# Optimization experiments

Hardware: AMD Instinct MI355X
Metric: run time of the kernel (lower is better)

Reference implementation:

```python
import math
import jax, jax.numpy as jnp
import numpy as np

C = 256
CQ = C // 8
B, H, W = 8, 64, 64


def setup_inputs() -> dict:
    key = jax.random.key(0)
    k1, k2, k3, k4 = jax.random.split(key, 4)
    x = jax.random.normal(k1, (B, C, H, W), dtype=jnp.float32)
    # 1x1 conv weights, bias=False -> plain [out, in] matrices
    wq = jax.random.normal(k2, (CQ, C), dtype=jnp.float32) * 0.02
    wk = jax.random.normal(k3, (CQ, C), dtype=jnp.float32) * 0.02
    wv = jax.random.normal(k4, (C, C), dtype=jnp.float32) * 0.02
    # gamma init is zeros in the torch module; use small nonzero so output depends on attention path
    gamma = jnp.ones((1,), dtype=jnp.float32) * 0.5
    return {"x": x, "wq": wq, "wk": wk, "wv": wv, "gamma": gamma}


def reference(x, wq, wk, wv, gamma):
    b, c, h, w = x.shape
    n = h * w
    xr = x.reshape(b, c, n)                       # [B, C, N]
    q = jnp.einsum('oc,bcn->bon', wq, xr)         # [B, Cq, N]
    k = jnp.einsum('oc,bcn->bon', wk, xr)         # [B, Cq, N]
    v = jnp.einsum('oc,bcn->bon', wv, xr)         # [B, C, N]
    # attn[b, i, j] = softmax_j( q[:, i] . k[:, j] / sqrt(Cq) )
    scores = jnp.einsum('bci,bcj->bij', q, k) / math.sqrt(q.shape[1])  # [B, N, N]
    attn = jax.nn.softmax(scores, axis=-1)
    # out[b, c, m] = sum_n v[b, c, n] * attn[b, m, n]
    out = jnp.einsum('bcn,bmn->bcm', v, attn).reshape(b, c, h, w)
    return gamma[0] * out + x
```

## Files before the change

kernel.cpp:

```cpp
#include <hip/hip_runtime.h>

#define B_ 8
#define C_ 256
#define CQ_ 32
#define N_ 4096

typedef __attribute__((ext_vector_type(8))) short short8;
typedef __attribute__((ext_vector_type(4))) float float4v;

#define QSCALE 0.2550599232f

#if __has_builtin(__builtin_amdgcn_exp2f)
#define EXP2F __builtin_amdgcn_exp2f
#else
#define EXP2F exp2f
#endif

static __device__ __forceinline__ unsigned short f2bf(float f) {
  unsigned int u = __float_as_uint(f);
  u += 0x7FFFu + ((u >> 16) & 1u);
  return (unsigned short)(u >> 16);
}

static __device__ __forceinline__ void async16(void* lds, const void* g) {
  __builtin_amdgcn_global_load_lds(
      (const __attribute__((address_space(1))) unsigned int*)g,
      (__attribute__((address_space(3))) unsigned int*)lds, 16, 0, 0);
}

__global__ __launch_bounds__(256) void wconv_kernel(
    const float* __restrict__ wq, const float* __restrict__ wk,
    const float* __restrict__ wv, unsigned short* __restrict__ w_bf) {
  int o = blockIdx.x * 8 + (threadIdx.x >> 5);
  int c8 = (threadIdx.x & 31) * 8;
  const float* src; float sc = 1.f;
  if (o < 32)      { src = wq + (size_t)o * 256; sc = QSCALE; }
  else if (o < 64) { src = wk + (size_t)(o - 32) * 256; }
  else             { src = wv + (size_t)(o - 64) * 256; }
  float4 a = *(const float4*)(src + c8);
  float4 bq = *(const float4*)(src + c8 + 4);
  unsigned short t[8] = {f2bf(a.x*sc), f2bf(a.y*sc), f2bf(a.z*sc), f2bf(a.w*sc),
                         f2bf(bq.x*sc), f2bf(bq.y*sc), f2bf(bq.z*sc), f2bf(bq.w*sc)};
  *(uint4*)(w_bf + (size_t)o * 256 + c8) = *(const uint4*)t;
}

__global__ __launch_bounds__(256, 2) void proj_kernel(
    const float* __restrict__ x, const unsigned short* __restrict__ w_bf,
    unsigned short* __restrict__ qT, unsigned short* __restrict__ kT,
    unsigned short* __restrict__ v) {
  __shared__ __align__(16) unsigned short xb[2][64 * 32];
  int tid = threadIdx.x, wave = tid >> 6, lane = tid & 63;
  int q16 = lane >> 4, l16 = lane & 15;
  int b = blockIdx.x, n0 = blockIdx.y * 64;

  int p = tid & 15, n4g = tid >> 4;
  const float* x0 = x + (size_t)b * C_ * N_ + n0 + n4g * 4;

  auto stage = [&](int buf, int ks) {
    const float* r0 = x0 + (size_t)(ks * 32 + 2 * p) * N_;
    float4 fa = *(const float4*)(r0);
    float4 fb = *(const float4*)(r0 + N_);
    float va[4] = {fa.x, fa.y, fa.z, fa.w};
    float vb[4] = {fb.x, fb.y, fb.z, fb.w};
    #pragma unroll
    for (int i = 0; i < 4; ++i) {
      int n = n4g * 4 + i;
      unsigned int pk = (unsigned int)f2bf(va[i]) | ((unsigned int)f2bf(vb[i]) << 16);
      int so = (p >> 2) ^ ((n >> 1) & 3);
      *(unsigned int*)(&xb[buf][n * 32 + so * 8 + (p & 3) * 2]) = pk;
    }
  };

  float4v acc[5][4];
  float4v zerov = {0.f, 0.f, 0.f, 0.f};
  #pragma unroll
  for (int mt = 0; mt < 5; ++mt)
    for (int nt = 0; nt < 4; ++nt) acc[mt][nt] = zerov;

  stage(0, 0);
  __syncthreads();

  int o0 = wave * 80;
  int sxo = (q16 ^ ((l16 >> 1) & 3)) * 8;
  #pragma unroll 1
  for (int ks = 0; ks < 8; ++ks) {
    if (ks < 7) stage((ks + 1) & 1, ks + 1);
    short8 af[5], bf4[4];
    #pragma unroll
    for (int mt = 0; mt < 5; ++mt)
      af[mt] = *(const short8*)(w_bf + (size_t)(o0 + mt * 16 + l16) * 256 + ks * 32 + q16 * 8);
    #pragma unroll
    for (int nt = 0; nt < 4; ++nt)
      bf4[nt] = *(const short8*)(&xb[ks & 1][(nt * 16 + l16) * 32 + sxo]);
    #pragma unroll
    for (int mt = 0; mt < 5; ++mt)
      #pragma unroll
      for (int nt = 0; nt < 4; ++nt)
        acc[mt][nt] = __builtin_amdgcn_mfma_f32_16x16x32_bf16(af[mt], bf4[nt], acc[mt][nt], 0, 0, 0);
    __syncthreads();
  }

  #pragma unroll
  for (int mt = 0; mt < 5; ++mt) {
    int og = o0 + mt * 16 + q16 * 4;
    #pragma unroll
    for (int nt = 0; nt < 4; ++nt) {
      int n = n0 + nt * 16 + l16;
      unsigned short t[4];
      if (og < 64) {
        #pragma unroll
        for (int r = 0; r < 4; ++r) t[r] = f2bf(acc[mt][nt][r]);
        unsigned short* dst = (og < 32) ? (qT + ((size_t)b * N_ + n) * CQ_ + og)
                                        : (kT + ((size_t)b * N_ + n) * CQ_ + (og - 32));
        *(uint2*)dst = *(const uint2*)t;
      } else {
        #pragma unroll
        for (int r = 0; r < 4; ++r)
          v[((size_t)b * C_ + og - 64 + r) * N_ + n] = f2bf(acc[mt][nt][r]);
      }
    }
  }
}

__global__ __launch_bounds__(256, 2) void attn_kernel(
    const unsigned short* __restrict__ qT, const unsigned short* __restrict__ kT,
    const unsigned short* __restrict__ v, const float* __restrict__ x,
    const float* __restrict__ gamma, float* __restrict__ out) {
  __shared__ __align__(16) unsigned short kt_lds[2][64 * 32];
  __shared__ __align__(16) unsigned short p_lds[2][64 * 64];
  __shared__ float l_lds[64];

  int tid = threadIdx.x, wave = tid >> 6, lane = tid & 63;
  int q16 = lane >> 4, l16 = lane & 15;
  int bid = blockIdx.x, b = bid & 7, m0 = (bid >> 3) * 64;

  short8 qfrag = *(const short8*)(qT + ((size_t)b * N_ + m0 + wave * 16 + l16) * CQ_ + q16 * 8);

  auto stageK = [&](int buf, int j0) {
    int r = wave * 16 + (lane >> 2);
    int lo = (lane & 3) ^ ((r >> 1) & 3);
    async16(&kt_lds[buf][wave * 16 * 32], kT + ((size_t)b * N_ + j0 + r) * CQ_ + lo * 8);
  };

  const unsigned short* vw = v + ((size_t)b * C_ + wave * 64) * N_;
  uint4 vfr[2][8];
  auto vload = [&](uint4* dst, int j0) {
    #pragma unroll
    for (int ks = 0; ks < 2; ++ks)
      #pragma unroll
      for (int ct = 0; ct < 4; ++ct)
        dst[ks * 4 + ct] =
            *(const uint4*)(vw + (size_t)(ct * 16 + l16) * N_ + j0 + ks * 32 + q16 * 8);
  };

  stageK(0, 0);
  __syncthreads();
  vload(vfr[0], 0);

  float4v acc[4][4];
  float4v zerov = {0.f, 0.f, 0.f, 0.f};
  #pragma unroll
  for (int mt = 0; mt < 4; ++mt)
    for (int ct = 0; ct < 4; ++ct) acc[mt][ct] = zerov;
  float lrun[4] = {0.f, 0.f, 0.f, 0.f};

  int kro = q16 ^ ((l16 >> 1) & 3);
  int vro = l16 & 7;
  int lo8 = l16 >> 3, li = l16 & 7;

  #pragma unroll 2
  for (int j = 0; j < 64; ++j) {
    int cur = j & 1;
    float4v s[4];
    #pragma unroll
    for (int jt = 0; jt < 4; ++jt) {
      short8 kf = *(const short8*)(&kt_lds[cur][(jt * 16 + l16) * 32 + kro * 8]);
      s[jt] = __builtin_amdgcn_mfma_f32_16x16x32_bf16(qfrag, kf, zerov, 0, 0, 0);
    }
    if (j < 63) stageK(cur ^ 1, (j + 1) * 64);

    #pragma unroll
    for (int r = 0; r < 4; ++r) {
      float p0 = EXP2F(s[0][r]), p1 = EXP2F(s[1][r]);
      float p2 = EXP2F(s[2][r]), p3 = EXP2F(s[3][r]);
      lrun[r] += (p0 + p1) + (p2 + p3);
      int prow = wave * 16 + q16 * 4 + r;
      int rl = (q16 * 4 + r) & 7;
      unsigned short* pr = &p_lds[cur][prow * 64 + li];
      int o0 = lo8 ^ rl;
      pr[(o0 ^ 0) * 8] = (unsigned short)(__float_as_uint(p0) >> 16);
      pr[(o0 ^ 2) * 8] = (unsigned short)(__float_as_uint(p1) >> 16);
      pr[(o0 ^ 4) * 8] = (unsigned short)(__float_as_uint(p2) >> 16);
      pr[(o0 ^ 6) * 8] = (unsigned short)(__float_as_uint(p3) >> 16);
    }
    if (j == 63) {
      #pragma unroll
      for (int r = 0; r < 4; ++r) {
        float t = lrun[r];
        t += __shfl_xor(t, 1); t += __shfl_xor(t, 2);
        t += __shfl_xor(t, 4); t += __shfl_xor(t, 8);
        if (l16 == 0) l_lds[wave * 16 + q16 * 4 + r] = t;
      }
    }
    __syncthreads();

    if (j < 63) vload(vfr[cur ^ 1], (j + 1) * 64);

    #pragma unroll
    for (int ks = 0; ks < 2; ++ks) {
      short8 pf[4];
      #pragma unroll
      for (int mt = 0; mt < 4; ++mt)
        pf[mt] = *(const short8*)(&p_lds[cur][(mt * 16 + l16) * 64 + ((ks * 4 + q16) ^ vro) * 8]);
      #pragma unroll
      for (int ct = 0; ct < 4; ++ct) {
        short8 vf = *(const short8*)&vfr[cur][ks * 4 + ct];
        #pragma unroll
        for (int mt = 0; mt < 4; ++mt)
          acc[mt][ct] = __builtin_amdgcn_mfma_f32_16x16x32_bf16(pf[mt], vf, acc[mt][ct], 0, 0, 0);
      }
    }
  }

  float g = gamma[0];
  #pragma unroll
  for (int mt = 0; mt < 4; ++mt) {
    float linv[4];
    #pragma unroll
    for (int r = 0; r < 4; ++r) linv[r] = 1.f / l_lds[mt * 16 + q16 * 4 + r];
    int n = m0 + mt * 16 + q16 * 4;
    #pragma unroll
    for (int ct = 0; ct < 4; ++ct) {
      int c = wave * 64 + ct * 16 + l16;
      size_t off = ((size_t)b * C_ + c) * N_ + n;
      float4 xv = *(const float4*)(x + off);
      float4 o;
      o.x = g * acc[mt][ct][0] * linv[0] + xv.x;
      o.y = g * acc[mt][ct][1] * linv[1] + xv.y;
      o.z = g * acc[mt][ct][2] * linv[2] + xv.z;
      o.w = g * acc[mt][ct][3] * linv[3] + xv.w;
      *(float4*)(out + off) = o;
    }
  }
}

extern "C" void kernel_launch(void* const* d_in, const int* in_sizes, int n_in,
                              void* d_out, int out_size, void* d_ws, size_t ws_size,
                              hipStream_t stream) {
  const float* x     = (const float*)d_in[0];
  const float* wq    = (const float*)d_in[1];
  const float* wk    = (const float*)d_in[2];
  const float* wv    = (const float*)d_in[3];
  const float* gamma = (const float*)d_in[4];
  float* out = (float*)d_out;

  unsigned short* qT  = (unsigned short*)d_ws;
  unsigned short* kT  = qT + (size_t)B_ * N_ * CQ_;
  unsigned short* vv  = kT + (size_t)B_ * N_ * CQ_;
  unsigned short* wbf = vv + (size_t)B_ * C_ * N_;

  hipLaunchKernelGGL(wconv_kernel, dim3(40), dim3(256), 0, stream, wq, wk, wv, wbf);
  hipLaunchKernelGGL(proj_kernel, dim3(8, 64), dim3(256), 0, stream, x, wbf, qT, kT, vv);
  hipLaunchKernelGGL(attn_kernel, dim3(512), dim3(256), 0, stream, qT, kT, vv, x, gamma, out);
}
```

Before: 228.6 us.

## Double attention block to 128 query rows with V staged in shared LDS

Each attention block now covers 128 query rows with 512 threads (8 waves), halving the grid. Each V tile is staged once into LDS via async copies and shared by both halves of the query rows, so V is fetched from global memory half as often as before, when every wave loaded its own V fragments into registers. In exchange the P buffer is single-buffered and a second __syncthreads per iteration guards the V and P LDS reuse, which serialises more of the loop. The larger LDS footprint and block size may also lower occupancy, and 256 blocks may underfill the GPU.

```diff
diff --git a/kernel.cpp b/kernel.cpp
--- a/kernel.cpp
+++ b/kernel.cpp
@@ -122,40 +122,42 @@
   }
 }
 
-__global__ __launch_bounds__(256, 2) void attn_kernel(
+__global__ __launch_bounds__(512, 2) void attn_kernel(
     const unsigned short* __restrict__ qT, const unsigned short* __restrict__ kT,
     const unsigned short* __restrict__ v, const float* __restrict__ x,
     const float* __restrict__ gamma, float* __restrict__ out) {
+  __shared__ __align__(16) unsigned short v_lds[256 * 64];
   __shared__ __align__(16) unsigned short kt_lds[2][64 * 32];
-  __shared__ __align__(16) unsigned short p_lds[2][64 * 64];
-  __shared__ float l_lds[64];
+  __shared__ __align__(16) unsigned short p_lds[128 * 64];
+  __shared__ float l_lds[128];
 
   int tid = threadIdx.x, wave = tid >> 6, lane = tid & 63;
   int q16 = lane >> 4, l16 = lane & 15;
-  int bid = blockIdx.x, b = bid & 7, m0 = (bid >> 3) * 64;
+  int bid = blockIdx.x, b = bid & 7, m0 = (bid >> 3) * 128;
 
   short8 qfrag = *(const short8*)(qT + ((size_t)b * N_ + m0 + wave * 16 + l16) * CQ_ + q16 * 8);
 
+  const unsigned short* vbase = v + (size_t)b * C_ * N_;
+  auto stageV = [&](int j0) {
+    #pragma unroll
+    for (int it = 0; it < 4; ++it) {
+      int r = wave * 32 + it * 8 + (lane >> 3);
+      int lo = (lane & 7) ^ (lane >> 3);
+      async16(&v_lds[(wave * 32 + it * 8) * 64], vbase + (size_t)r * N_ + j0 + lo * 8);
+    }
+  };
   auto stageK = [&](int buf, int j0) {
-    int r = wave * 16 + (lane >> 2);
-    int lo = (lane & 3) ^ ((r >> 1) & 3);
-    async16(&kt_lds[buf][wave * 16 * 32], kT + ((size_t)b * N_ + j0 + r) * CQ_ + lo * 8);
+    if (wave >= 4) {
+      int w4 = wave - 4;
+      int r = w4 * 16 + (lane >> 2);
+      int lo = (lane & 3) ^ ((r >> 1) & 3);
+      async16(&kt_lds[buf][w4 * 16 * 32], kT + ((size_t)b * N_ + j0 + r) * CQ_ + lo * 8);
+    }
   };
 
-  const unsigned short* vw = v + ((size_t)b * C_ + wave * 64) * N_;
-  uint4 vfr[2][8];
-  auto vload = [&](uint4* dst, int j0) {
-    #pragma unroll
-    for (int ks = 0; ks < 2; ++ks)
-      #pragma unroll
-      for (int ct = 0; ct < 4; ++ct)
-        dst[ks * 4 + ct] =
-            *(const uint4*)(vw + (size_t)(ct * 16 + l16) * N_ + j0 + ks * 32 + q16 * 8);
-  };
-
   stageK(0, 0);
+  stageV(0);
   __syncthreads();
-  vload(vfr[0], 0);
 
   float4v acc[4][4];
   float4v zerov = {0.f, 0.f, 0.f, 0.f};
@@ -167,8 +169,8 @@
   int kro = q16 ^ ((l16 >> 1) & 3);
   int vro = l16 & 7;
   int lo8 = l16 >> 3, li = l16 & 7;
-
-  #pragma unroll 2
+  int h = wave >> 2, cq = wave & 3;
+
   for (int j = 0; j < 64; ++j) {
     int cur = j & 1;
     float4v s[4];
@@ -177,7 +179,6 @@
       short8 kf = *(const short8*)(&kt_lds[cur][(jt * 16 + l16) * 32 + kro * 8]);
       s[jt] = __builtin_amdgcn_mfma_f32_16x16x32_bf16(qfrag, kf, zerov, 0, 0, 0);
     }
-    if (j < 63) stageK(cur ^ 1, (j + 1) * 64);
 
     #pragma unroll
     for (int r = 0; r < 4; ++r) {
@@ -186,7 +187,7 @@
       lrun[r] += (p0 + p1) + (p2 + p3);
       int prow = wave * 16 + q16 * 4 + r;
       int rl = (q16 * 4 + r) & 7;
-      unsigned short* pr = &p_lds[cur][prow * 64 + li];
+      unsigned short* pr = &p_lds[prow * 64 + li];
       int o0 = lo8 ^ rl;
       pr[(o0 ^ 0) * 8] = (unsigned short)(__float_as_uint(p0) >> 16);
       pr[(o0 ^ 2) * 8] = (unsigned short)(__float_as_uint(p1) >> 16);
@@ -204,22 +205,26 @@
     }
     __syncthreads();
 
-    if (j < 63) vload(vfr[cur ^ 1], (j + 1) * 64);
+    if (j < 63) stageK(cur ^ 1, (j + 1) * 64);
 
     #pragma unroll
     for (int ks = 0; ks < 2; ++ks) {
-      short8 pf[4];
+      short8 pf[4], vf[4];
       #pragma unroll
       for (int mt = 0; mt < 4; ++mt)
-        pf[mt] = *(const short8*)(&p_lds[cur][(mt * 16 + l16) * 64 + ((ks * 4 + q16) ^ vro) * 8]);
-      #pragma unroll
-      for (int ct = 0; ct < 4; ++ct) {
-        short8 vf = *(const short8*)&vfr[cur][ks * 4 + ct];
+        pf[mt] = *(const short8*)(&p_lds[(h * 64 + mt * 16 + l16) * 64 + ((ks * 4 + q16) ^ vro) * 8]);
+      #pragma unroll
+      for (int ct = 0; ct < 4; ++ct)
+        vf[ct] = *(const short8*)(&v_lds[(cq * 64 + ct * 16 + l16) * 64 + ((ks * 4 + q16) ^ vro) * 8]);
+      #pragma unroll
+      for (int mt = 0; mt < 4; ++mt)
         #pragma unroll
-        for (int mt = 0; mt < 4; ++mt)
-          acc[mt][ct] = __builtin_amdgcn_mfma_f32_16x16x32_bf16(pf[mt], vf, acc[mt][ct], 0, 0, 0);
-      }
-    }
+        for (int ct = 0; ct < 4; ++ct)
+          acc[mt][ct] = __builtin_amdgcn_mfma_f32_16x16x32_bf16(pf[mt], vf[ct], acc[mt][ct], 0, 0, 0);
+    }
+    __syncthreads();
+
+    if (j < 63) stageV((j + 1) * 64);
   }
 
   float g = gamma[0];
@@ -227,11 +232,11 @@
   for (int mt = 0; mt < 4; ++mt) {
     float linv[4];
     #pragma unroll
-    for (int r = 0; r < 4; ++r) linv[r] = 1.f / l_lds[mt * 16 + q16 * 4 + r];
-    int n = m0 + mt * 16 + q16 * 4;
+    for (int r = 0; r < 4; ++r) linv[r] = 1.f / l_lds[h * 64 + mt * 16 + q16 * 4 + r];
+    int n = m0 + h * 64 + mt * 16 + q16 * 4;
     #pragma unroll
     for (int ct = 0; ct < 4; ++ct) {
-      int c = wave * 64 + ct * 16 + l16;
+      int c = cq * 64 + ct * 16 + l16;
       size_t off = ((size_t)b * C_ + c) * N_ + n;
       float4 xv = *(const float4*)(x + off);
       float4 o;
@@ -261,5 +266,5 @@
 
   hipLaunchKernelGGL(wconv_kernel, dim3(40), dim3(256), 0, stream, wq, wk, wv, wbf);
   hipLaunchKernelGGL(proj_kernel, dim3(8, 64), dim3(256), 0, stream, x, wbf, qT, kT, vv);
-  hipLaunchKernelGGL(attn_kernel, dim3(512), dim3(256), 0, stream, qT, kT, vv, x, gamma, out);
-}
+  hipLaunchKernelGGL(attn_kernel, dim3(256), dim3(512), 0, stream, qT, kT, vv, x, gamma, out);
+}
```

Result: faster. 192.1 us (-16.0%).
